# Kernel optimization log

Measured on AMD Instinct MI355X. Metric: run time of the kernel, lower is better.

Reference implementation:

```python
import jax, jax.numpy as jnp
import numpy as np

N_NODES = 100000
N_EDGES = 1600000
D = 128
BETA = 0.001
EPS = 1e-12  # F.normalize eps


def setup_inputs() -> dict:
    key = jax.random.key(0)
    k1, k2, k3, k4, k5, k6 = jax.random.split(key, 6)
    stdv = 1.0 / np.sqrt(D)
    return {
        "input": jax.random.normal(k1, (N_NODES, D), dtype=jnp.float32),
        "edge_rows": jax.random.randint(k2, (N_EDGES,), 0, N_NODES, dtype=jnp.int32),
        "edge_cols": jax.random.randint(k3, (N_EDGES,), 0, N_NODES, dtype=jnp.int32),
        "edge_vals": jax.random.uniform(k4, (N_EDGES,), dtype=jnp.float32),
        "weight": jax.random.uniform(k5, (D, D), minval=-stdv, maxval=stdv, dtype=jnp.float32),
        "bias": jax.random.uniform(k6, (D,), minval=-stdv, maxval=stdv, dtype=jnp.float32),
    }


def reference(input, edge_rows, edge_cols, edge_vals, weight, bias):
    # dense projection: [N, D]
    support = input @ weight
    # sparse neighbor aggregation: agg[i] = sum_{(i,j) in E} adj_val * support[j]
    msgs = edge_vals[:, None] * support[edge_cols]          # [E, D]
    agg = jax.ops.segment_sum(msgs, edge_rows, num_segments=input.shape[0])
    # beta-weighted residual blend
    out = BETA * input + (1.0 - BETA) * agg
    # row-wise L2 normalize (torch F.normalize, p=2, dim=1)
    norm = jnp.sqrt(jnp.sum(out * out, axis=1, keepdims=True))
    out = out / jnp.maximum(norm, EPS)
    # bias add
    return out + bias
```

## Files before the change

kernel.cpp:

```cpp
#include <hip/hip_runtime.h>

#define N_NODES 100000
#define N_EDGES 1600000
#define D 128
#define NB 1563
#define NSUB 8
#define SUBCAP 224
#define CAP (NSUB*SUBCAP)
#define STAGE 1536

typedef short bf16x8 __attribute__((ext_vector_type(8)));
typedef float f32x4 __attribute__((ext_vector_type(4)));

__device__ __forceinline__ unsigned short f2bf(float x){
  union { float f; unsigned u; } v; v.f = x;
  unsigned r = v.u + 0x7fffu + ((v.u >> 16) & 1u);
  return (unsigned short)(r >> 16);
}

__device__ __forceinline__ float bf2f(unsigned short h){
  union { unsigned u; float f; } v; v.u = ((unsigned)h) << 16;
  return v.f;
}

__global__ __launch_bounds__(256) void convert_input(const float4* __restrict__ in4,
                                                     ushort4* __restrict__ outb){
  int i = blockIdx.x*256 + threadIdx.x;
  float4 a = in4[i];
  ushort4 h;
  h.x = f2bf(a.x); h.y = f2bf(a.y); h.z = f2bf(a.z); h.w = f2bf(a.w);
  outb[i] = h;
}

__global__ __launch_bounds__(256) void scatter_direct(const int* __restrict__ rows,
                                                      const int* __restrict__ cols,
                                                      const float* __restrict__ vals,
                                                      int* __restrict__ cursor,
                                                      int2* __restrict__ edges_s){
  int i = blockIdx.x*256 + threadIdx.x;
  int s = blockIdx.x & (NSUB-1);
  int r = rows[i];
  int b = r >> 6;
  int pos = atomicAdd(&cursor[s*NB + b], 1);
  if (pos < SUBCAP)
    edges_s[(size_t)b*CAP + s*SUBCAP + pos] =
        make_int2(cols[i] | ((r & 63) << 17), __float_as_int(vals[i]));
}

__global__ __launch_bounds__(256) void sortB_kernel(int2* __restrict__ edges,
                                                    const int* __restrict__ cursor,
                                                    int* __restrict__ row_start,
                                                    int* __restrict__ counts){
  __shared__ int2 st[STAGE];
  __shared__ int hist[64];
  __shared__ int cur[64];
  int t = threadIdx.x;
  int b = blockIdx.x;
  int base = b * CAP;
  if (t < 64) hist[t] = 0;
  __syncthreads();
  int off = 0;
  #pragma unroll
  for (int s = 0; s < NSUB; ++s){
    int ms = cursor[s*NB + b];
    if (ms > SUBCAP) ms = SUBCAP;
    for (int i = t; i < ms; i += 256){
      int2 e = edges[base + s*SUBCAP + i];
      st[off + i] = e;
      atomicAdd(&hist[((unsigned)e.x) >> 17], 1);
    }
    off += ms;
  }
  int m = off;
  __syncthreads();
  if (t < 64){
    int c = hist[t];
    int x = c;
    #pragma unroll
    for (int o = 1; o < 64; o <<= 1){
      int y = __shfl_up(x, o);
      if (t >= o) x += y;
    }
    int excl = x - c;
    cur[t] = excl;
    int grow = b*64 + t;
    row_start[grow] = base + excl;
    counts[grow] = c;
  }
  __syncthreads();
  for (int i = t; i < m; i += 256){
    int2 e = st[i];
    int r = ((unsigned)e.x) >> 17;
    int pos = atomicAdd(&cur[r], 1);
    edges[base + pos] = make_int2(e.x & 0x1FFFF, e.y);
  }
}

__global__ void transpose_w(const float* __restrict__ W, unsigned short* __restrict__ WT){
  int idx = blockIdx.x*256 + threadIdx.x;
  int k = idx >> 7, c = idx & 127;
  WT[c*128 + k] = f2bf(W[idx]);
}

__global__ __launch_bounds__(256) void agg_kernel(const ushort4* __restrict__ inb4,
                                                  const int* __restrict__ row_start,
                                                  const int* __restrict__ counts,
                                                  const int2* __restrict__ edges,
                                                  ushort4* __restrict__ aggb){
  int g = threadIdx.x >> 5, l = threadIdx.x & 31;
  int row = blockIdx.x*8 + g;
  int start = row_start[row];
  int n = counts[row];
  int e = start, end = start + n;

  float4 a0 = make_float4(0.f,0.f,0.f,0.f);
  float4 a1 = make_float4(0.f,0.f,0.f,0.f);
  float4 a2 = make_float4(0.f,0.f,0.f,0.f);
  float4 a3 = make_float4(0.f,0.f,0.f,0.f);

  for (; e + 4 <= end; e += 4){
    int2 e0 = edges[e+0];
    int2 e1 = edges[e+1];
    int2 e2 = edges[e+2];
    int2 e3 = edges[e+3];
    ushort4 x0 = inb4[(size_t)e0.x*32 + l];
    ushort4 x1 = inb4[(size_t)e1.x*32 + l];
    ushort4 x2 = inb4[(size_t)e2.x*32 + l];
    ushort4 x3 = inb4[(size_t)e3.x*32 + l];
    float v0 = __int_as_float(e0.y), v1 = __int_as_float(e1.y);
    float v2 = __int_as_float(e2.y), v3 = __int_as_float(e3.y);
    a0.x = fmaf(v0, bf2f(x0.x), a0.x); a0.y = fmaf(v0, bf2f(x0.y), a0.y);
    a0.z = fmaf(v0, bf2f(x0.z), a0.z); a0.w = fmaf(v0, bf2f(x0.w), a0.w);
    a1.x = fmaf(v1, bf2f(x1.x), a1.x); a1.y = fmaf(v1, bf2f(x1.y), a1.y);
    a1.z = fmaf(v1, bf2f(x1.z), a1.z); a1.w = fmaf(v1, bf2f(x1.w), a1.w);
    a2.x = fmaf(v2, bf2f(x2.x), a2.x); a2.y = fmaf(v2, bf2f(x2.y), a2.y);
    a2.z = fmaf(v2, bf2f(x2.z), a2.z); a2.w = fmaf(v2, bf2f(x2.w), a2.w);
    a3.x = fmaf(v3, bf2f(x3.x), a3.x); a3.y = fmaf(v3, bf2f(x3.y), a3.y);
    a3.z = fmaf(v3, bf2f(x3.z), a3.z); a3.w = fmaf(v3, bf2f(x3.w), a3.w);
  }
  for (; e < end; ++e){
    int2 ee = edges[e];
    ushort4 x = inb4[(size_t)ee.x*32 + l];
    float v = __int_as_float(ee.y);
    a0.x = fmaf(v, bf2f(x.x), a0.x); a0.y = fmaf(v, bf2f(x.y), a0.y);
    a0.z = fmaf(v, bf2f(x.z), a0.z); a0.w = fmaf(v, bf2f(x.w), a0.w);
  }
  float4 s;
  s.x = (a0.x + a1.x) + (a2.x + a3.x);
  s.y = (a0.y + a1.y) + (a2.y + a3.y);
  s.z = (a0.z + a1.z) + (a2.z + a3.z);
  s.w = (a0.w + a1.w) + (a2.w + a3.w);
  ushort4 h;
  h.x = f2bf(s.x); h.y = f2bf(s.y); h.z = f2bf(s.z); h.w = f2bf(s.w);
  aggb[(size_t)row*32 + l] = h;
}

__global__ __launch_bounds__(256) void final_kernel(const ushort4* __restrict__ aggb,
                                                    const float* __restrict__ input,
                                                    const unsigned short* __restrict__ WT,
                                                    const float* __restrict__ bias,
                                                    float* __restrict__ out){
  __shared__ unsigned short Ws[128*136];
  __shared__ unsigned short As[64*136];
  int t = threadIdx.x;
  int block_row = blockIdx.x * 64;

  const ushort4* WT4 = (const ushort4*)WT;
  #pragma unroll
  for (int i = 0; i < 16; ++i){
    int idx4 = i*256 + t;
    int c = idx4 >> 5, k4 = idx4 & 31;
    ushort4 w = WT4[idx4];
    *((ushort4*)&Ws[c*136 + k4*4]) = w;
  }
  #pragma unroll
  for (int i = 0; i < 8; ++i){
    int idx4 = i*256 + t;
    int row = idx4 >> 5, k4 = idx4 & 31;
    int grow = block_row + row;
    ushort4 h = make_ushort4(0,0,0,0);
    if (grow < N_NODES) h = aggb[(size_t)grow*32 + k4];
    *((ushort4*)&As[row*136 + k4*4]) = h;
  }
  __syncthreads();

  int wave = t >> 6, lane = t & 63;
  int q = lane >> 4, n = lane & 15;

  bf16x8 afr[4];
  #pragma unroll
  for (int ks = 0; ks < 4; ++ks)
    afr[ks] = *((const bf16x8*)&As[(wave*16 + n)*136 + ks*32 + q*8]);

  f32x4 acc[8];
  #pragma unroll
  for (int ct = 0; ct < 8; ++ct) acc[ct] = (f32x4){0.f, 0.f, 0.f, 0.f};

  #pragma unroll
  for (int ct = 0; ct < 8; ++ct){
    #pragma unroll
    for (int ks = 0; ks < 4; ++ks){
      bf16x8 bfr = *((const bf16x8*)&Ws[(ct*16 + n)*136 + ks*32 + q*8]);
      acc[ct] = __builtin_amdgcn_mfma_f32_16x16x32_bf16(afr[ks], bfr, acc[ct], 0, 0, 0);
    }
  }

  int base_row = block_row + wave*16 + q*4;
  float v[8][4];
  float s[4] = {0.f, 0.f, 0.f, 0.f};
  #pragma unroll
  for (int reg = 0; reg < 4; ++reg){
    int grow = base_row + reg;
    const float* inrow = input + (size_t)grow * D;
    #pragma unroll
    for (int ct = 0; ct < 8; ++ct){
      float inp = (grow < N_NODES) ? inrow[ct*16 + n] : 0.f;
      float val = fmaf(0.999f, acc[ct][reg], 0.001f * inp);
      v[ct][reg] = val;
      s[reg] = fmaf(val, val, s[reg]);
    }
  }
  #pragma unroll
  for (int reg = 0; reg < 4; ++reg){
    float x = s[reg];
    x += __shfl_xor(x, 1);
    x += __shfl_xor(x, 2);
    x += __shfl_xor(x, 4);
    x += __shfl_xor(x, 8);
    s[reg] = x;
  }
  #pragma unroll
  for (int reg = 0; reg < 4; ++reg){
    int grow = base_row + reg;
    if (grow >= N_NODES) continue;
    float scale = 1.f / fmaxf(sqrtf(s[reg]), 1e-12f);
    float* outrow = out + (size_t)grow * D;
    #pragma unroll
    for (int ct = 0; ct < 8; ++ct){
      outrow[ct*16 + n] = fmaf(v[ct][reg], scale, bias[ct*16 + n]);
    }
  }
}

extern "C" void kernel_launch(void* const* d_in, const int* in_sizes, int n_in,
                              void* d_out, int out_size, void* d_ws, size_t ws_size,
                              hipStream_t stream){
  const float* input  = (const float*)d_in[0];
  const int*   erows  = (const int*)d_in[1];
  const int*   ecols  = (const int*)d_in[2];
  const float* evals  = (const float*)d_in[3];
  const float* weight = (const float*)d_in[4];
  const float* bias   = (const float*)d_in[5];
  float* out = (float*)d_out;

  int*   cursor    = (int*)d_ws;
  int*   row_start = cursor + NSUB*NB;
  int*   counts    = row_start + NB*64;
  int2*  edges_s   = (int2*)(counts + NB*64);
  ushort4* aggb    = (ushort4*)(edges_s + (size_t)NB*CAP);
  ushort4* inb     = aggb + (size_t)N_NODES * 32;
  unsigned short* WTg = (unsigned short*)(inb + (size_t)N_NODES * 32);

  hipMemsetAsync(cursor, 0, NSUB * NB * sizeof(int), stream);
  convert_input<<<12500, 256, 0, stream>>>((const float4*)input, inb);
  scatter_direct<<<N_EDGES/256, 256, 0, stream>>>(erows, ecols, evals, cursor, edges_s);
  sortB_kernel<<<NB, 256, 0, stream>>>(edges_s, cursor, row_start, counts);
  transpose_w<<<64, 256, 0, stream>>>(weight, WTg);
  agg_kernel<<<N_NODES/8, 256, 0, stream>>>(inb, row_start, counts, edges_s, aggb);
  final_kernel<<<(N_NODES + 63)/64, 256, 0, stream>>>(aggb, input, WTg, bias, out);
}
```

Baseline: 325.9 us.

## Fuse per-bucket edge sort into aggregation kernel and read residual from bf16 input

Merges the shared-memory bucket sort into the aggregation kernel so sorted edges stay in LDS and are consumed directly by waves that grab rows dynamically, removing a kernel launch and a global write/read of the edge array. The cursor memset is folded into the input conversion kernel, and the final kernel reads the residual input from the bf16 copy instead of fp32. It trades fewer, larger aggregation blocks (lower parallelism) and slight residual precision loss for reduced memory traffic and launch overhead.

```diff
diff --git a/kernel.cpp b/kernel.cpp
--- a/kernel.cpp
+++ b/kernel.cpp
@@ -24,8 +24,10 @@
 }
 
 __global__ __launch_bounds__(256) void convert_input(const float4* __restrict__ in4,
-                                                     ushort4* __restrict__ outb){
+                                                     ushort4* __restrict__ outb,
+                                                     int* __restrict__ cursor){
   int i = blockIdx.x*256 + threadIdx.x;
+  if (i < NSUB*NB) cursor[i] = 0;
   float4 a = in4[i];
   ushort4 h;
   h.x = f2bf(a.x); h.y = f2bf(a.y); h.z = f2bf(a.z); h.w = f2bf(a.w);
@@ -47,116 +49,127 @@
         make_int2(cols[i] | ((r & 63) << 17), __float_as_int(vals[i]));
 }
 
-__global__ __launch_bounds__(256) void sortB_kernel(int2* __restrict__ edges,
-                                                    const int* __restrict__ cursor,
-                                                    int* __restrict__ row_start,
-                                                    int* __restrict__ counts){
-  __shared__ int2 st[STAGE];
-  __shared__ int hist[64];
-  __shared__ int cur[64];
-  int t = threadIdx.x;
-  int b = blockIdx.x;
-  int base = b * CAP;
-  if (t < 64) hist[t] = 0;
-  __syncthreads();
-  int off = 0;
-  #pragma unroll
-  for (int s = 0; s < NSUB; ++s){
-    int ms = cursor[s*NB + b];
-    if (ms > SUBCAP) ms = SUBCAP;
-    for (int i = t; i < ms; i += 256){
-      int2 e = edges[base + s*SUBCAP + i];
-      st[off + i] = e;
-      atomicAdd(&hist[((unsigned)e.x) >> 17], 1);
-    }
-    off += ms;
-  }
-  int m = off;
-  __syncthreads();
-  if (t < 64){
-    int c = hist[t];
-    int x = c;
-    #pragma unroll
-    for (int o = 1; o < 64; o <<= 1){
-      int y = __shfl_up(x, o);
-      if (t >= o) x += y;
-    }
-    int excl = x - c;
-    cur[t] = excl;
-    int grow = b*64 + t;
-    row_start[grow] = base + excl;
-    counts[grow] = c;
-  }
-  __syncthreads();
-  for (int i = t; i < m; i += 256){
-    int2 e = st[i];
-    int r = ((unsigned)e.x) >> 17;
-    int pos = atomicAdd(&cur[r], 1);
-    edges[base + pos] = make_int2(e.x & 0x1FFFF, e.y);
-  }
-}
-
 __global__ void transpose_w(const float* __restrict__ W, unsigned short* __restrict__ WT){
   int idx = blockIdx.x*256 + threadIdx.x;
   int k = idx >> 7, c = idx & 127;
   WT[c*128 + k] = f2bf(W[idx]);
 }
 
-__global__ __launch_bounds__(256) void agg_kernel(const ushort4* __restrict__ inb4,
-                                                  const int* __restrict__ row_start,
-                                                  const int* __restrict__ counts,
-                                                  const int2* __restrict__ edges,
-                                                  ushort4* __restrict__ aggb){
-  int g = threadIdx.x >> 5, l = threadIdx.x & 31;
-  int row = blockIdx.x*8 + g;
-  int start = row_start[row];
-  int n = counts[row];
-  int e = start, end = start + n;
-
-  float4 a0 = make_float4(0.f,0.f,0.f,0.f);
-  float4 a1 = make_float4(0.f,0.f,0.f,0.f);
-  float4 a2 = make_float4(0.f,0.f,0.f,0.f);
-  float4 a3 = make_float4(0.f,0.f,0.f,0.f);
-
-  for (; e + 4 <= end; e += 4){
-    int2 e0 = edges[e+0];
-    int2 e1 = edges[e+1];
-    int2 e2 = edges[e+2];
-    int2 e3 = edges[e+3];
-    ushort4 x0 = inb4[(size_t)e0.x*32 + l];
-    ushort4 x1 = inb4[(size_t)e1.x*32 + l];
-    ushort4 x2 = inb4[(size_t)e2.x*32 + l];
-    ushort4 x3 = inb4[(size_t)e3.x*32 + l];
-    float v0 = __int_as_float(e0.y), v1 = __int_as_float(e1.y);
-    float v2 = __int_as_float(e2.y), v3 = __int_as_float(e3.y);
-    a0.x = fmaf(v0, bf2f(x0.x), a0.x); a0.y = fmaf(v0, bf2f(x0.y), a0.y);
-    a0.z = fmaf(v0, bf2f(x0.z), a0.z); a0.w = fmaf(v0, bf2f(x0.w), a0.w);
-    a1.x = fmaf(v1, bf2f(x1.x), a1.x); a1.y = fmaf(v1, bf2f(x1.y), a1.y);
-    a1.z = fmaf(v1, bf2f(x1.z), a1.z); a1.w = fmaf(v1, bf2f(x1.w), a1.w);
-    a2.x = fmaf(v2, bf2f(x2.x), a2.x); a2.y = fmaf(v2, bf2f(x2.y), a2.y);
-    a2.z = fmaf(v2, bf2f(x2.z), a2.z); a2.w = fmaf(v2, bf2f(x2.w), a2.w);
-    a3.x = fmaf(v3, bf2f(x3.x), a3.x); a3.y = fmaf(v3, bf2f(x3.y), a3.y);
-    a3.z = fmaf(v3, bf2f(x3.z), a3.z); a3.w = fmaf(v3, bf2f(x3.w), a3.w);
-  }
-  for (; e < end; ++e){
-    int2 ee = edges[e];
-    ushort4 x = inb4[(size_t)ee.x*32 + l];
-    float v = __int_as_float(ee.y);
-    a0.x = fmaf(v, bf2f(x.x), a0.x); a0.y = fmaf(v, bf2f(x.y), a0.y);
-    a0.z = fmaf(v, bf2f(x.z), a0.z); a0.w = fmaf(v, bf2f(x.w), a0.w);
-  }
-  float4 s;
-  s.x = (a0.x + a1.x) + (a2.x + a3.x);
-  s.y = (a0.y + a1.y) + (a2.y + a3.y);
-  s.z = (a0.z + a1.z) + (a2.z + a3.z);
-  s.w = (a0.w + a1.w) + (a2.w + a3.w);
-  ushort4 h;
-  h.x = f2bf(s.x); h.y = f2bf(s.y); h.z = f2bf(s.z); h.w = f2bf(s.w);
-  aggb[(size_t)row*32 + l] = h;
+__global__ __launch_bounds__(256) void agg_fused(const ushort4* __restrict__ inb4,
+                                                 const int* __restrict__ cursor,
+                                                 const int2* __restrict__ edges_g,
+                                                 ushort4* __restrict__ aggb){
+  __shared__ int2 st[STAGE];
+  __shared__ int hist[64];
+  __shared__ int cur[64];
+  __shared__ int rs[64];
+  __shared__ int rc[64];
+  __shared__ int rowctr;
+  int t = threadIdx.x;
+  int b = blockIdx.x;
+  size_t base = (size_t)b * CAP;
+
+  if (t < 64) hist[t] = 0;
+  if (t == 0) rowctr = 0;
+  __syncthreads();
+
+  int2 held[NSUB];
+  int hv = 0;
+  #pragma unroll
+  for (int s = 0; s < NSUB; ++s){
+    int ms = cursor[s*NB + b];
+    if (ms > SUBCAP) ms = SUBCAP;
+    if (t < ms){
+      int2 e = edges_g[base + s*SUBCAP + t];
+      held[s] = e;
+      hv |= (1 << s);
+      atomicAdd(&hist[((unsigned)e.x) >> 17], 1);
+    }
+  }
+  __syncthreads();
+
+  if (t < 64){
+    int c = hist[t];
+    int x = c;
+    #pragma unroll
+    for (int o = 1; o < 64; o <<= 1){
+      int y = __shfl_up(x, o);
+      if (t >= o) x += y;
+    }
+    int excl = x - c;
+    cur[t] = excl;
+    rs[t] = excl;
+    rc[t] = c;
+  }
+  __syncthreads();
+
+  #pragma unroll
+  for (int s = 0; s < NSUB; ++s){
+    if (hv & (1 << s)){
+      int2 e = held[s];
+      int r = ((unsigned)e.x) >> 17;
+      int pos = atomicAdd(&cur[r], 1);
+      st[pos] = make_int2(e.x & 0x1FFFF, e.y);
+    }
+  }
+  __syncthreads();
+
+  int l = t & 31;
+  for (;;){
+    int r = 0;
+    if (l == 0) r = atomicAdd(&rowctr, 1);
+    r = __shfl(r, 0, 32);
+    if (r >= 64) break;
+
+    int e = rs[r], end = e + rc[r];
+    float4 a0 = make_float4(0.f,0.f,0.f,0.f);
+    float4 a1 = make_float4(0.f,0.f,0.f,0.f);
+    float4 a2 = make_float4(0.f,0.f,0.f,0.f);
+    float4 a3 = make_float4(0.f,0.f,0.f,0.f);
+
+    for (; e + 4 <= end; e += 4){
+      int2 e0 = st[e+0];
+      int2 e1 = st[e+1];
+      int2 e2 = st[e+2];
+      int2 e3 = st[e+3];
+      ushort4 x0 = inb4[(size_t)e0.x*32 + l];
+      ushort4 x1 = inb4[(size_t)e1.x*32 + l];
+      ushort4 x2 = inb4[(size_t)e2.x*32 + l];
+      ushort4 x3 = inb4[(size_t)e3.x*32 + l];
+      float v0 = __int_as_float(e0.y), v1 = __int_as_float(e1.y);
+      float v2 = __int_as_float(e2.y), v3 = __int_as_float(e3.y);
+      a0.x = fmaf(v0, bf2f(x0.x), a0.x); a0.y = fmaf(v0, bf2f(x0.y), a0.y);
+      a0.z = fmaf(v0, bf2f(x0.z), a0.z); a0.w = fmaf(v0, bf2f(x0.w), a0.w);
+      a1.x = fmaf(v1, bf2f(x1.x), a1.x); a1.y = fmaf(v1, bf2f(x1.y), a1.y);
+      a1.z = fmaf(v1, bf2f(x1.z), a1.z); a1.w = fmaf(v1, bf2f(x1.w), a1.w);
+      a2.x = fmaf(v2, bf2f(x2.x), a2.x); a2.y = fmaf(v2, bf2f(x2.y), a2.y);
+      a2.z = fmaf(v2, bf2f(x2.z), a2.z); a2.w = fmaf(v2, bf2f(x2.w), a2.w);
+      a3.x = fmaf(v3, bf2f(x3.x), a3.x); a3.y = fmaf(v3, bf2f(x3.y), a3.y);
+      a3.z = fmaf(v3, bf2f(x3.z), a3.z); a3.w = fmaf(v3, bf2f(x3.w), a3.w);
+    }
+    for (; e < end; ++e){
+      int2 ee = st[e];
+      ushort4 x = inb4[(size_t)ee.x*32 + l];
+      float v = __int_as_float(ee.y);
+      a0.x = fmaf(v, bf2f(x.x), a0.x); a0.y = fmaf(v, bf2f(x.y), a0.y);
+      a0.z = fmaf(v, bf2f(x.z), a0.z); a0.w = fmaf(v, bf2f(x.w), a0.w);
+    }
+    float4 s;
+    s.x = (a0.x + a1.x) + (a2.x + a3.x);
+    s.y = (a0.y + a1.y) + (a2.y + a3.y);
+    s.z = (a0.z + a1.z) + (a2.z + a3.z);
+    s.w = (a0.w + a1.w) + (a2.w + a3.w);
+    int grow = b*64 + r;
+    if (grow < N_NODES){
+      ushort4 h;
+      h.x = f2bf(s.x); h.y = f2bf(s.y); h.z = f2bf(s.z); h.w = f2bf(s.w);
+      aggb[(size_t)grow*32 + l] = h;
+    }
+  }
 }
 
 __global__ __launch_bounds__(256) void final_kernel(const ushort4* __restrict__ aggb,
-                                                    const float* __restrict__ input,
+                                                    const unsigned short* __restrict__ inb,
                                                     const unsigned short* __restrict__ WT,
                                                     const float* __restrict__ bias,
                                                     float* __restrict__ out){
@@ -211,10 +224,10 @@
   #pragma unroll
   for (int reg = 0; reg < 4; ++reg){
     int grow = base_row + reg;
-    const float* inrow = input + (size_t)grow * D;
+    const unsigned short* inrow = inb + (size_t)grow * D;
     #pragma unroll
     for (int ct = 0; ct < 8; ++ct){
-      float inp = (grow < N_NODES) ? inrow[ct*16 + n] : 0.f;
+      float inp = (grow < N_NODES) ? bf2f(inrow[ct*16 + n]) : 0.f;
       float val = fmaf(0.999f, acc[ct][reg], 0.001f * inp);
       v[ct][reg] = val;
       s[reg] = fmaf(val, val, s[reg]);
@@ -254,18 +267,15 @@
   float* out = (float*)d_out;
 
   int*   cursor    = (int*)d_ws;
-  int*   row_start = cursor + NSUB*NB;
-  int*   counts    = row_start + NB*64;
-  int2*  edges_s   = (int2*)(counts + NB*64);
+  int2*  edges_s   = (int2*)(cursor + NSUB*NB);
   ushort4* aggb    = (ushort4*)(edges_s + (size_t)NB*CAP);
   ushort4* inb     = aggb + (size_t)N_NODES * 32;
   unsigned short* WTg = (unsigned short*)(inb + (size_t)N_NODES * 32);
 
-  hipMemsetAsync(cursor, 0, NSUB * NB * sizeof(int), stream);
-  convert_input<<<12500, 256, 0, stream>>>((const float4*)input, inb);
+  convert_input<<<12500, 256, 0, stream>>>((const float4*)input, inb, cursor);
   scatter_direct<<<N_EDGES/256, 256, 0, stream>>>(erows, ecols, evals, cursor, edges_s);
-  sortB_kernel<<<NB, 256, 0, stream>>>(edges_s, cursor, row_start, counts);
   transpose_w<<<64, 256, 0, stream>>>(weight, WTg);
-  agg_kernel<<<N_NODES/8, 256, 0, stream>>>(inb, row_start, counts, edges_s, aggb);
-  final_kernel<<<(N_NODES + 63)/64, 256, 0, stream>>>(aggb, input, WTg, bias, out);
-}
+  agg_fused<<<NB, 256, 0, stream>>>((const ushort4*)inb, cursor, edges_s, aggb);
+  final_kernel<<<(N_NODES + 63)/64, 256, 0, stream>>>(aggb, (const unsigned short*)inb,
+                                                      WTg, bias, out);
+}
```

New measurement: 315.6 us. 3.2% less time.
